# Optimization experiments

Hardware: AMD Instinct MI355X
Metric: run time of the kernel (lower is better)

The kernel has to match this reference:

```python
import jax, jax.numpy as jnp
import numpy as np

GATE_DIM = 1313 + 622  # hardcoded in the module
D1 = 300
D2 = 300
OUT = 300


def setup_inputs() -> dict:
    key = jax.random.key(0)
    ks = jax.random.split(key, 12)
    N, M = 384, 384
    inp = {
        "feature1": jax.random.normal(ks[0], (N, GATE_DIM), jnp.float32),
        "box1": jax.random.uniform(ks[1], (N, 5), jnp.float32),
        "feature2": jax.random.normal(ks[2], (M, GATE_DIM), jnp.float32),
        "box2": jax.random.uniform(ks[3], (M, 5), jnp.float32),
        "attrlabel_embeddings": jax.random.normal(ks[4], (GATE_DIM, D1), jnp.float32) * 0.05,
        # learned parameters
        "gate1": 10.0 * jnp.ones((GATE_DIM,), jnp.float32),
        "gate2": 10.0 * jnp.ones((GATE_DIM,), jnp.float32),
        "weight_loc": jnp.zeros((2,), jnp.float32),
        "fc1_w": jax.random.normal(ks[5], (OUT, D1 + D2), jnp.float32) * (1.0 / np.sqrt(D1 + D2)),
        "fc1_b": jnp.zeros((OUT,), jnp.float32),
        "fc2_w": jax.random.normal(ks[6], (OUT, 10), jnp.float32) * (1.0 / np.sqrt(10.0)),
        "fc2_b": jnp.zeros((OUT,), jnp.float32),
        "fc3_w": jax.random.normal(ks[7], (OUT, OUT), jnp.float32) * (1.0 / np.sqrt(OUT)),
        "fc3_b": jnp.zeros((OUT,), jnp.float32),
    }
    return inp


def _preprocess(feature, box):
    # repo's preprocess callable; modeled as identity on the feature
    # (feature already has dim input_dim1/input_dim2 expected by fc1)
    return feature


def reference(feature1, box1, feature2, box2, attrlabel_embeddings,
              gate1, gate2, weight_loc,
              fc1_w, fc1_b, fc2_w, fc2_b, fc3_w, fc3_b):
    # gated feature -> attrlabel embedding projection
    f1 = (feature1 * jax.nn.sigmoid(gate1)) @ attrlabel_embeddings  # [N, D1]
    f1 = _preprocess(f1, box1)
    f2 = (feature2 * jax.nn.sigmoid(gate2)) @ attrlabel_embeddings  # [M, D2]
    f2 = _preprocess(f2, box2)

    # fc1(cat(meshgrid(f1,f2))) == f1@W_a^T (broadcast over M) + f2@W_b^T (broadcast over N) + b
    Wa, Wb = fc1_w[:, :f1.shape[-1]], fc1_w[:, f1.shape[-1]:]
    semantic = jax.nn.relu(
        jnp.einsum('nd,od->no', f1, Wa)[:, None, :]
        + jnp.einsum('md,od->mo', f2, Wb)[None, :, :]
        + fc1_b
    )  # [N, M, OUT]

    Wa2, Wb2 = fc2_w[:, :5], fc2_w[:, 5:]
    spatial = jax.nn.relu(
        jnp.einsum('nd,od->no', box1, Wa2)[:, None, :]
        + jnp.einsum('md,od->mo', box2, Wb2)[None, :, :]
        + fc2_b
    )  # [N, M, OUT]

    w = jax.nn.softmax(weight_loc)
    mixed = w[0] * semantic + w[1] * spatial
    embedding = jnp.einsum('nmo,po->nmp', mixed, fc3_w) + fc3_b  # [N, M, OUT]
    return embedding
```

## Files before the change

### kernel.cpp

```cpp
#include <hip/hip_runtime.h>
#include <hip/hip_bf16.h>

#define NROW 384
#define GD   1935
#define GK   1952
#define DD   300
#define KP   320
#define DP   304

#define OFF_SIG1 0
#define OFF_SIG2 2048
#define OFF_W    4096
#define OFF_XBF  4112
#define OFF_EBT  753680
#define OFF_FC1B 1066000
#define OFF_FC3B 1168400
#define OFF_F1B  1217040
#define OFF_AB   1339920
#define OFF_CD   1585680

typedef short short8 __attribute__((ext_vector_type(8)));
typedef float floatx4 __attribute__((ext_vector_type(4)));

__device__ inline unsigned short f2bf(float x){
  union { float f; unsigned u; } v; v.f = x;
  unsigned r = v.u + 0x7fffu + ((v.u >> 16) & 1u);
  return (unsigned short)(r >> 16);
}

__global__ void k_prep(const float* g1, const float* g2, const float* wloc, float* ws){
  int t = blockIdx.x * 256 + threadIdx.x;
  if (t < GD) ws[OFF_SIG1 + t] = 1.f / (1.f + expf(-g1[t]));
  else if (t < 2*GD) ws[OFF_SIG2 + t - GD] = 1.f / (1.f + expf(-g2[t - GD]));
  else if (t == 2*GD){
    float a = wloc[0], b = wloc[1];
    float m = fmaxf(a, b);
    float ea = expf(a - m), eb = expf(b - m);
    ws[OFF_W + 0] = ea / (ea + eb);
    ws[OFF_W + 1] = eb / (ea + eb);
  }
}

#define NX  (2*384*GK)
#define NE  (KP*GK)
#define NF1 (2*KP*KP)
#define NF3 (DP*KP)
__global__ void k_cvt_all(const float* f1, const float* f2, const float* E,
                          const float* fc1w, const float* fc3w, float* ws){
  int t = blockIdx.x * 256 + threadIdx.x;
  unsigned short* xbf  = (unsigned short*)(ws + OFF_XBF);
  unsigned short* ebt  = (unsigned short*)(ws + OFF_EBT);
  unsigned short* f1b  = (unsigned short*)(ws + OFF_FC1B);
  unsigned short* f3b  = (unsigned short*)(ws + OFF_FC3B);
  if (t < NX){
    int z = t / (384*GK); int r = t - z*384*GK;
    int n = r / GK, k = r - n*GK;
    const float* X   = z ? f2 : f1;
    const float* sig = ws + (z ? OFF_SIG2 : OFF_SIG1);
    float v = (k < GD) ? X[n*GD + k] * sig[k] : 0.f;
    xbf[t] = f2bf(v);
  } else if (t < NX + NE){
    int r = t - NX;
    int c = r / GK, k = r - c*GK;
    float v = (k < GD && c < DD) ? E[k*DD + c] : 0.f;
    ebt[r] = f2bf(v);
  } else if (t < NX + NE + NF1){
    int r = t - NX - NE;
    int z = r / (KP*KP); int r2 = r - z*KP*KP;
    int o = r2 / KP, d = r2 - o*KP;
    float v = (o < DD && d < DD) ? fc1w[o*(2*DD) + z*DD + d] : 0.f;
    f1b[r] = f2bf(v);
  } else {
    int r = t - NX - NE - NF1;
    int p = r / KP, k = r - p*KP;
    float v = (p < DD && k < DD) ? fc3w[p*DD + k] : 0.f;
    f3b[r] = f2bf(v);
  }
}

__global__ __launch_bounds__(256) void k_gg(float* ws){
  int z = blockIdx.y;
  const unsigned short* X   = (const unsigned short*)(ws + OFF_XBF) + z*384*GK;
  const unsigned short* Ebt = (const unsigned short*)(ws + OFF_EBT);
  unsigned short* out       = (unsigned short*)(ws + OFF_F1B) + z*384*KP;
  int t = threadIdx.x, lane = t & 63;
  int id = blockIdx.x * 4 + (t >> 6);
  int mt = id / 20, ct = id - mt*20;
  int col = lane & 15, quad = lane >> 4;
  const unsigned short* ap = X   + (mt*16 + col)*GK + quad*8;
  const unsigned short* bp = Ebt + (ct*16 + col)*GK + quad*8;
  floatx4 acc = (floatx4){0.f,0.f,0.f,0.f};
  for (int kc = 0; kc < 61; ++kc){
    short8 a = *(const short8*)(ap + kc*32);
    short8 b = *(const short8*)(bp + kc*32);
    acc = __builtin_amdgcn_mfma_f32_16x16x32_bf16(a, b, acc, 0, 0, 0);
  }
  int c = ct*16 + col;
  #pragma unroll
  for (int r = 0; r < 4; ++r){
    int m = mt*16 + quad*4 + r;
    out[m*KP + c] = (c < DD) ? f2bf(acc[r]) : (unsigned short)0;
  }
}

__global__ __launch_bounds__(256) void k_sem(const float* fc1b, float* ws){
  int z = blockIdx.y;
  const unsigned short* F = (const unsigned short*)(ws + OFF_F1B) + z*384*KP;
  const unsigned short* W = (const unsigned short*)(ws + OFF_FC1B) + z*KP*KP;
  float* out = ws + OFF_AB + z*384*KP;
  float w0 = ws[OFF_W];
  int t = threadIdx.x, lane = t & 63;
  int id = blockIdx.x * 4 + (t >> 6);
  int rt = id / 20, ot = id - rt*20;
  int col = lane & 15, quad = lane >> 4;
  const unsigned short* ap = F + (rt*16 + col)*KP + quad*8;
  const unsigned short* bp = W + (ot*16 + col)*KP + quad*8;
  floatx4 acc = (floatx4){0.f,0.f,0.f,0.f};
  #pragma unroll
  for (int kc = 0; kc < 10; ++kc){
    short8 a = *(const short8*)(ap + kc*32);
    short8 b = *(const short8*)(bp + kc*32);
    acc = __builtin_amdgcn_mfma_f32_16x16x32_bf16(a, b, acc, 0, 0, 0);
  }
  int o = ot*16 + col;
  float bias = (z == 0 && o < DD) ? fc1b[o] : 0.f;
  #pragma unroll
  for (int r = 0; r < 4; ++r){
    int rr = rt*16 + quad*4 + r;
    out[rr*KP + o] = (o < DD) ? w0 * (acc[r] + bias) : 0.f;
  }
}

__global__ void k_spa(const float* box1, const float* box2, const float* fc2w,
                      const float* fc2b, float* ws){
  int z = blockIdx.y;
  const float* bx = z ? box2 : box1;
  float* out = ws + OFF_CD + z*384*KP;
  int joff = z ? 5 : 0;
  float w1 = ws[OFF_W + 1];
  int t = blockIdx.x * 256 + threadIdx.x;
  int r = t / KP, o = t - r*KP;
  float v = 0.f;
  if (o < DD){
    const float* b = bx + r * 5;
    const float* wr = fc2w + o * 10 + joff;
    v = b[0]*wr[0] + b[1]*wr[1] + b[2]*wr[2] + b[3]*wr[3] + b[4]*wr[4];
    if (!z) v += fc2b[o];
    v *= w1;
  }
  out[t] = v;
}

__global__ __launch_bounds__(512, 4) void k_main(const float* fc3b, float* out, const float* ws){
  __shared__ __align__(16) unsigned short smix[512 * 8];
  __shared__ __align__(16) unsigned short swt[1216 * 8];
  const unsigned short* fc3bf = (const unsigned short*)(ws + OFF_FC3B);
  int t = threadIdx.x;
  int lane = t & 63, wave = t >> 6;
  int col = lane & 15, quad = lane >> 4;
  int mt0 = blockIdx.x * 128;
  int n = blockIdx.y;
  const float* Ah = ws + OFF_AB + n * KP;
  const float* Bh = ws + OFF_AB + 384 * KP;
  const float* Ch = ws + OFF_CD + n * KP;
  const float* Dh = ws + OFF_CD + 384 * KP;

  floatx4 acc[19];
  #pragma unroll
  for (int i = 0; i < 19; ++i) acc[i] = (floatx4){0.f,0.f,0.f,0.f};

  int w_b  = t >> 6;
  int j    = (t >> 4) & 3;
  int colb = t & 15;
  int mg = mt0 + w_b*16 + colb;
  const float* pB = Bh + (size_t)mg * KP;
  const float* pD = Dh + (size_t)mg * KP;

  for (int kc = 0; kc < 10; ++kc){
    int kb = kc*32 + j*8;
    {
      union { unsigned short s[8]; uint4 v; } u;
      float4 a0 = *(const float4*)(Ah + kb);
      float4 c0 = *(const float4*)(Ch + kb);
      float4 b0 = *(const float4*)(pB + kb);
      float4 d0 = *(const float4*)(pD + kb);
      u.s[0] = f2bf(fmaxf(a0.x + b0.x, 0.f) + fmaxf(c0.x + d0.x, 0.f));
      u.s[1] = f2bf(fmaxf(a0.y + b0.y, 0.f) + fmaxf(c0.y + d0.y, 0.f));
      u.s[2] = f2bf(fmaxf(a0.z + b0.z, 0.f) + fmaxf(c0.z + d0.z, 0.f));
      u.s[3] = f2bf(fmaxf(a0.w + b0.w, 0.f) + fmaxf(c0.w + d0.w, 0.f));
      float4 a1 = *(const float4*)(Ah + kb + 4);
      float4 c1 = *(const float4*)(Ch + kb + 4);
      float4 b1 = *(const float4*)(pB + kb + 4);
      float4 d1 = *(const float4*)(pD + kb + 4);
      u.s[4] = f2bf(fmaxf(a1.x + b1.x, 0.f) + fmaxf(c1.x + d1.x, 0.f));
      u.s[5] = f2bf(fmaxf(a1.y + b1.y, 0.f) + fmaxf(c1.y + d1.y, 0.f));
      u.s[6] = f2bf(fmaxf(a1.z + b1.z, 0.f) + fmaxf(c1.z + d1.z, 0.f));
      u.s[7] = f2bf(fmaxf(a1.w + b1.w, 0.f) + fmaxf(c1.w + d1.w, 0.f));
      *(uint4*)&smix[t * 8] = u.v;
    }
    for (int s = t; s < 1216; s += 512){
      int pt = s >> 6, l = s & 63;
      int cc = l & 15, qq = l >> 4;
      uint4 w = *(const uint4*)(fc3bf + (pt*16 + cc)*KP + kc*32 + qq*8);
      *(uint4*)&swt[s * 8] = w;
    }
    __syncthreads();
    short8 af = *(const short8*)&smix[(wave*64 + lane) * 8];
    #pragma unroll
    for (int pt = 0; pt < 19; ++pt){
      short8 bf = *(const short8*)&swt[(pt*64 + lane) * 8];
      acc[pt] = __builtin_amdgcn_mfma_f32_16x16x32_bf16(af, bf, acc[pt], 0, 0, 0);
    }
    __syncthreads();
  }

  #pragma unroll
  for (int pt = 0; pt < 19; ++pt){
    int p = pt*16 + col;
    if (p < DD){
      float bias = fc3b[p];
      #pragma unroll
      for (int r = 0; r < 4; ++r){
        int m = mt0 + wave*16 + quad*4 + r;
        out[((size_t)n * NROW + m) * DD + p] = acc[pt][r] + bias;
      }
    }
  }
}

extern "C" void kernel_launch(void* const* d_in, const int* in_sizes, int n_in,
                              void* d_out, int out_size, void* d_ws, size_t ws_size,
                              hipStream_t stream) {
  const float* feature1 = (const float*)d_in[0];
  const float* box1     = (const float*)d_in[1];
  const float* feature2 = (const float*)d_in[2];
  const float* box2     = (const float*)d_in[3];
  const float* E        = (const float*)d_in[4];
  const float* gate1    = (const float*)d_in[5];
  const float* gate2    = (const float*)d_in[6];
  const float* wloc     = (const float*)d_in[7];
  const float* fc1w     = (const float*)d_in[8];
  const float* fc1b     = (const float*)d_in[9];
  const float* fc2w     = (const float*)d_in[10];
  const float* fc2b     = (const float*)d_in[11];
  const float* fc3w     = (const float*)d_in[12];
  const float* fc3b     = (const float*)d_in[13];
  float* out = (float*)d_out;
  float* ws  = (float*)d_ws;

  hipLaunchKernelGGL(k_prep, dim3(16), dim3(256), 0, stream, gate1, gate2, wloc, ws);
  hipLaunchKernelGGL(k_cvt_all, dim3((NX+NE+NF1+NF3)/256), dim3(256), 0, stream,
                     feature1, feature2, E, fc1w, fc3w, ws);
  hipLaunchKernelGGL(k_gg, dim3(120, 2), dim3(256), 0, stream, ws);
  hipLaunchKernelGGL(k_sem, dim3(120, 2), dim3(256), 0, stream, fc1b, ws);
  hipLaunchKernelGGL(k_spa, dim3(480, 2), dim3(256), 0, stream,
                     box1, box2, fc2w, fc2b, ws);
  hipLaunchKernelGGL(k_main, dim3(3, NROW), dim3(512), 0, stream, fc3b, out, ws);
}
```

Before: 334.3 us.

## Split-K small GEMMs across waves, fuse sigmoid into convert, double-buffer main kernel

Several changes land together. The gate sigmoid is now computed inline in the convert kernel, which removes its separate workspace pass. The k_gg and k_sem GEMMs split K across four waves per block and reduce the partial sums through shared memory, giving four times as many blocks for better occupancy. k_main drops the shared mix buffer: each wave builds its A fragment in registers and the fc3 weight tiles are double-buffered, so the next stage loads while MFMAs run, with one barrier per iteration. The trade is more shared memory, more registers and some redundant sigmoid evaluation.

```diff
diff --git a/kernel.cpp b/kernel.cpp
--- a/kernel.cpp
+++ b/kernel.cpp
@@ -8,8 +8,6 @@
 #define KP   320
 #define DP   304
 
-#define OFF_SIG1 0
-#define OFF_SIG2 2048
 #define OFF_W    4096
 #define OFF_XBF  4112
 #define OFF_EBT  753680
@@ -28,11 +26,8 @@
   return (unsigned short)(r >> 16);
 }
 
-__global__ void k_prep(const float* g1, const float* g2, const float* wloc, float* ws){
-  int t = blockIdx.x * 256 + threadIdx.x;
-  if (t < GD) ws[OFF_SIG1 + t] = 1.f / (1.f + expf(-g1[t]));
-  else if (t < 2*GD) ws[OFF_SIG2 + t - GD] = 1.f / (1.f + expf(-g2[t - GD]));
-  else if (t == 2*GD){
+__global__ void k_prep(const float* wloc, float* ws){
+  if (threadIdx.x == 0){
     float a = wloc[0], b = wloc[1];
     float m = fmaxf(a, b);
     float ea = expf(a - m), eb = expf(b - m);
@@ -46,6 +41,7 @@
 #define NF1 (2*KP*KP)
 #define NF3 (DP*KP)
 __global__ void k_cvt_all(const float* f1, const float* f2, const float* E,
+                          const float* g1, const float* g2,
                           const float* fc1w, const float* fc3w, float* ws){
   int t = blockIdx.x * 256 + threadIdx.x;
   unsigned short* xbf  = (unsigned short*)(ws + OFF_XBF);
@@ -55,9 +51,13 @@
   if (t < NX){
     int z = t / (384*GK); int r = t - z*384*GK;
     int n = r / GK, k = r - n*GK;
-    const float* X   = z ? f2 : f1;
-    const float* sig = ws + (z ? OFF_SIG2 : OFF_SIG1);
-    float v = (k < GD) ? X[n*GD + k] * sig[k] : 0.f;
+    const float* X = z ? f2 : f1;
+    const float* g = z ? g2 : g1;
+    float v = 0.f;
+    if (k < GD){
+      float sig = 1.f / (1.f + __expf(-g[k]));
+      v = X[n*GD + k] * sig;
+    }
     xbf[t] = f2bf(v);
   } else if (t < NX + NE){
     int r = t - NX;
@@ -83,23 +83,32 @@
   const unsigned short* X   = (const unsigned short*)(ws + OFF_XBF) + z*384*GK;
   const unsigned short* Ebt = (const unsigned short*)(ws + OFF_EBT);
   unsigned short* out       = (unsigned short*)(ws + OFF_F1B) + z*384*KP;
-  int t = threadIdx.x, lane = t & 63;
-  int id = blockIdx.x * 4 + (t >> 6);
+  int t = threadIdx.x, lane = t & 63, w = t >> 6;
+  int id = blockIdx.x;
   int mt = id / 20, ct = id - mt*20;
   int col = lane & 15, quad = lane >> 4;
   const unsigned short* ap = X   + (mt*16 + col)*GK + quad*8;
   const unsigned short* bp = Ebt + (ct*16 + col)*GK + quad*8;
   floatx4 acc = (floatx4){0.f,0.f,0.f,0.f};
-  for (int kc = 0; kc < 61; ++kc){
+  #pragma unroll 4
+  for (int kc = w; kc < 61; kc += 4){
     short8 a = *(const short8*)(ap + kc*32);
     short8 b = *(const short8*)(bp + kc*32);
     acc = __builtin_amdgcn_mfma_f32_16x16x32_bf16(a, b, acc, 0, 0, 0);
   }
-  int c = ct*16 + col;
-  #pragma unroll
-  for (int r = 0; r < 4; ++r){
-    int m = mt*16 + quad*4 + r;
-    out[m*KP + c] = (c < DD) ? f2bf(acc[r]) : (unsigned short)0;
+  __shared__ __align__(16) float red[4][64][4];
+  *(floatx4*)&red[w][lane][0] = acc;
+  __syncthreads();
+  if (w == 0){
+    floatx4 s = *(floatx4*)&red[0][lane][0];
+    #pragma unroll
+    for (int i = 1; i < 4; ++i) s += *(floatx4*)&red[i][lane][0];
+    int c = ct*16 + col;
+    #pragma unroll
+    for (int r = 0; r < 4; ++r){
+      int m = mt*16 + quad*4 + r;
+      out[m*KP + c] = (c < DD) ? f2bf(s[r]) : (unsigned short)0;
+    }
   }
 }
 
@@ -109,25 +118,33 @@
   const unsigned short* W = (const unsigned short*)(ws + OFF_FC1B) + z*KP*KP;
   float* out = ws + OFF_AB + z*384*KP;
   float w0 = ws[OFF_W];
-  int t = threadIdx.x, lane = t & 63;
-  int id = blockIdx.x * 4 + (t >> 6);
+  int t = threadIdx.x, lane = t & 63, w = t >> 6;
+  int id = blockIdx.x;
   int rt = id / 20, ot = id - rt*20;
   int col = lane & 15, quad = lane >> 4;
   const unsigned short* ap = F + (rt*16 + col)*KP + quad*8;
   const unsigned short* bp = W + (ot*16 + col)*KP + quad*8;
   floatx4 acc = (floatx4){0.f,0.f,0.f,0.f};
   #pragma unroll
-  for (int kc = 0; kc < 10; ++kc){
+  for (int kc = w; kc < 10; kc += 4){
     short8 a = *(const short8*)(ap + kc*32);
     short8 b = *(const short8*)(bp + kc*32);
     acc = __builtin_amdgcn_mfma_f32_16x16x32_bf16(a, b, acc, 0, 0, 0);
   }
-  int o = ot*16 + col;
-  float bias = (z == 0 && o < DD) ? fc1b[o] : 0.f;
-  #pragma unroll
-  for (int r = 0; r < 4; ++r){
-    int rr = rt*16 + quad*4 + r;
-    out[rr*KP + o] = (o < DD) ? w0 * (acc[r] + bias) : 0.f;
+  __shared__ __align__(16) float red[4][64][4];
+  *(floatx4*)&red[w][lane][0] = acc;
+  __syncthreads();
+  if (w == 0){
+    floatx4 s = *(floatx4*)&red[0][lane][0];
+    #pragma unroll
+    for (int i = 1; i < 4; ++i) s += *(floatx4*)&red[i][lane][0];
+    int o = ot*16 + col;
+    float bias = (z == 0 && o < DD) ? fc1b[o] : 0.f;
+    #pragma unroll
+    for (int r = 0; r < 4; ++r){
+      int rr = rt*16 + quad*4 + r;
+      out[rr*KP + o] = (o < DD) ? w0 * (s[r] + bias) : 0.f;
+    }
   }
 }
 
@@ -152,8 +169,7 @@
 }
 
 __global__ __launch_bounds__(512, 4) void k_main(const float* fc3b, float* out, const float* ws){
-  __shared__ __align__(16) unsigned short smix[512 * 8];
-  __shared__ __align__(16) unsigned short swt[1216 * 8];
+  __shared__ __align__(16) unsigned short swt[2][1216 * 8];
   const unsigned short* fc3bf = (const unsigned short*)(ws + OFF_FC3B);
   int t = threadIdx.x;
   int lane = t & 63, wave = t >> 6;
@@ -165,52 +181,59 @@
   const float* Ch = ws + OFF_CD + n * KP;
   const float* Dh = ws + OFF_CD + 384 * KP;
 
+  int mg = mt0 + wave*16 + col;
+  const float* pB = Bh + (size_t)mg * KP;
+  const float* pD = Dh + (size_t)mg * KP;
+
   floatx4 acc[19];
   #pragma unroll
   for (int i = 0; i < 19; ++i) acc[i] = (floatx4){0.f,0.f,0.f,0.f};
 
-  int w_b  = t >> 6;
-  int j    = (t >> 4) & 3;
-  int colb = t & 15;
-  int mg = mt0 + w_b*16 + colb;
-  const float* pB = Bh + (size_t)mg * KP;
-  const float* pD = Dh + (size_t)mg * KP;
-
-  for (int kc = 0; kc < 10; ++kc){
-    int kb = kc*32 + j*8;
-    {
-      union { unsigned short s[8]; uint4 v; } u;
-      float4 a0 = *(const float4*)(Ah + kb);
-      float4 c0 = *(const float4*)(Ch + kb);
-      float4 b0 = *(const float4*)(pB + kb);
-      float4 d0 = *(const float4*)(pD + kb);
-      u.s[0] = f2bf(fmaxf(a0.x + b0.x, 0.f) + fmaxf(c0.x + d0.x, 0.f));
-      u.s[1] = f2bf(fmaxf(a0.y + b0.y, 0.f) + fmaxf(c0.y + d0.y, 0.f));
-      u.s[2] = f2bf(fmaxf(a0.z + b0.z, 0.f) + fmaxf(c0.z + d0.z, 0.f));
-      u.s[3] = f2bf(fmaxf(a0.w + b0.w, 0.f) + fmaxf(c0.w + d0.w, 0.f));
-      float4 a1 = *(const float4*)(Ah + kb + 4);
-      float4 c1 = *(const float4*)(Ch + kb + 4);
-      float4 b1 = *(const float4*)(pB + kb + 4);
-      float4 d1 = *(const float4*)(pD + kb + 4);
-      u.s[4] = f2bf(fmaxf(a1.x + b1.x, 0.f) + fmaxf(c1.x + d1.x, 0.f));
-      u.s[5] = f2bf(fmaxf(a1.y + b1.y, 0.f) + fmaxf(c1.y + d1.y, 0.f));
-      u.s[6] = f2bf(fmaxf(a1.z + b1.z, 0.f) + fmaxf(c1.z + d1.z, 0.f));
-      u.s[7] = f2bf(fmaxf(a1.w + b1.w, 0.f) + fmaxf(c1.w + d1.w, 0.f));
-      *(uint4*)&smix[t * 8] = u.v;
-    }
+  auto stage = [&](int buf, int kc){
+    #pragma unroll
     for (int s = t; s < 1216; s += 512){
       int pt = s >> 6, l = s & 63;
       int cc = l & 15, qq = l >> 4;
       uint4 w = *(const uint4*)(fc3bf + (pt*16 + cc)*KP + kc*32 + qq*8);
-      *(uint4*)&swt[s * 8] = w;
-    }
-    __syncthreads();
-    short8 af = *(const short8*)&smix[(wave*64 + lane) * 8];
+      *(uint4*)&swt[buf][s * 8] = w;
+    }
+  };
+  auto build = [&](int kc) -> short8 {
+    int kb = kc*32 + quad*8;
+    float4 a0 = *(const float4*)(Ah + kb),     a1 = *(const float4*)(Ah + kb + 4);
+    float4 c0 = *(const float4*)(Ch + kb),     c1 = *(const float4*)(Ch + kb + 4);
+    float4 b0 = *(const float4*)(pB + kb),     b1 = *(const float4*)(pB + kb + 4);
+    float4 d0 = *(const float4*)(pD + kb),     d1 = *(const float4*)(pD + kb + 4);
+    union { unsigned short s[8]; short8 v; } u;
+    u.s[0] = f2bf(fmaxf(a0.x + b0.x, 0.f) + fmaxf(c0.x + d0.x, 0.f));
+    u.s[1] = f2bf(fmaxf(a0.y + b0.y, 0.f) + fmaxf(c0.y + d0.y, 0.f));
+    u.s[2] = f2bf(fmaxf(a0.z + b0.z, 0.f) + fmaxf(c0.z + d0.z, 0.f));
+    u.s[3] = f2bf(fmaxf(a0.w + b0.w, 0.f) + fmaxf(c0.w + d0.w, 0.f));
+    u.s[4] = f2bf(fmaxf(a1.x + b1.x, 0.f) + fmaxf(c1.x + d1.x, 0.f));
+    u.s[5] = f2bf(fmaxf(a1.y + b1.y, 0.f) + fmaxf(c1.y + d1.y, 0.f));
+    u.s[6] = f2bf(fmaxf(a1.z + b1.z, 0.f) + fmaxf(c1.z + d1.z, 0.f));
+    u.s[7] = f2bf(fmaxf(a1.w + b1.w, 0.f) + fmaxf(c1.w + d1.w, 0.f));
+    return u.v;
+  };
+
+  stage(0, 0);
+  short8 af = build(0);
+  __syncthreads();
+
+  #pragma unroll 2
+  for (int kc = 0; kc < 10; ++kc){
+    int cur = kc & 1;
+    short8 afn = af;
+    if (kc < 9){
+      stage(1 - cur, kc + 1);
+      afn = build(kc + 1);
+    }
     #pragma unroll
     for (int pt = 0; pt < 19; ++pt){
-      short8 bf = *(const short8*)&swt[(pt*64 + lane) * 8];
+      short8 bf = *(const short8*)&swt[cur][(pt*64 + lane) * 8];
       acc[pt] = __builtin_amdgcn_mfma_f32_16x16x32_bf16(af, bf, acc[pt], 0, 0, 0);
     }
+    af = afn;
     __syncthreads();
   }
 
@@ -248,12 +271,12 @@
   float* out = (float*)d_out;
   float* ws  = (float*)d_ws;
 
-  hipLaunchKernelGGL(k_prep, dim3(16), dim3(256), 0, stream, gate1, gate2, wloc, ws);
+  hipLaunchKernelGGL(k_prep, dim3(1), dim3(64), 0, stream, wloc, ws);
   hipLaunchKernelGGL(k_cvt_all, dim3((NX+NE+NF1+NF3)/256), dim3(256), 0, stream,
-                     feature1, feature2, E, fc1w, fc3w, ws);
-  hipLaunchKernelGGL(k_gg, dim3(120, 2), dim3(256), 0, stream, ws);
-  hipLaunchKernelGGL(k_sem, dim3(120, 2), dim3(256), 0, stream, fc1b, ws);
+                     feature1, feature2, E, gate1, gate2, fc1w, fc3w, ws);
+  hipLaunchKernelGGL(k_gg, dim3(480, 2), dim3(256), 0, stream, ws);
   hipLaunchKernelGGL(k_spa, dim3(480, 2), dim3(256), 0, stream,
                      box1, box2, fc2w, fc2b, ws);
+  hipLaunchKernelGGL(k_sem, dim3(480, 2), dim3(256), 0, stream, fc1b, ws);
   hipLaunchKernelGGL(k_main, dim3(3, NROW), dim3(512), 0, stream, fc3b, out, ws);
 }
```

Result: no change. 335.9 us (+0.5%).
